# Kernel optimization log

Measured on AMD Instinct MI355X. Metric: run time of the kernel, lower is better.

Reference implementation:

```python
import jax, jax.numpy as jnp
import numpy as np

D = 64       # CNF state dimension
H = 512      # MLP hidden width
B = 8192     # batch


def setup_inputs() -> dict:
    key = jax.random.key(0)
    ks = jax.random.split(key, 8)
    s1 = 1.0 / np.sqrt(D + 1)
    s2 = 1.0 / np.sqrt(H)
    return {
        "t": jax.random.uniform(ks[0], (1,), dtype=jnp.float32),
        "x": jax.random.normal(ks[1], (B, D + 1), dtype=jnp.float32),
        "W1": jax.random.normal(ks[2], (D + 1, H), dtype=jnp.float32) * s1,
        "b1": jnp.zeros((H,), dtype=jnp.float32),
        "W2": jax.random.normal(ks[3], (H, H), dtype=jnp.float32) * s2,
        "b2": jnp.zeros((H,), dtype=jnp.float32),
        "W3": jax.random.normal(ks[4], (H, D), dtype=jnp.float32) * s2,
        "b3": jnp.zeros((D,), dtype=jnp.float32),
    }


def reference(t, x, W1, b1, W2, b2, W3, b3):
    # CNF.forward: strip log-density channel, evaluate vf and its exact divergence.
    xs = x[..., :-1]                      # [B, D]
    tt = t[0]

    def vf_single(xi):                    # xi: [D] -> [D]
        inp = jnp.concatenate([tt[None], xi])          # vf(t*ones, x) with t prepended
        h = jnp.tanh(inp @ W1 + b1)
        h = jnp.tanh(h @ W2 + b2)
        return h @ W3 + b3

    dx = jax.vmap(vf_single)(xs)                        # [B, D]
    # exact divergence: trace of per-sample Jacobian via reverse-mode (matches torch jacrev)
    J = jax.vmap(jax.jacrev(vf_single))(xs)             # [B, D, D]
    div = jnp.trace(J, axis1=-2, axis2=-1)              # [B]
    return jnp.concatenate([dx, div[:, None]], axis=-1) # [B, D+1]
```

## Files before the change

kernel.cpp:

```cpp
#include <hip/hip_runtime.h>

#define HH 512
#define DD 64
#define MROWS 32
#define TPB 512
#define LP 520

typedef unsigned short u16;
typedef short s16x8 __attribute__((ext_vector_type(8)));
typedef float f32x4 __attribute__((ext_vector_type(4)));

#define MFMA16(A,B,C) __builtin_amdgcn_mfma_f32_16x16x32_bf16((A),(B),(C),0,0,0)

#define OFF_EF   0
#define OFF_W2F  (HH*HH)
#define OFF_W1F  (2*HH*HH)
#define OFF_W3F  (2*HH*HH + HH*DD)
#define OFF_Z0B  ((2*HH*HH + 2*HH*DD)*2)

__device__ __forceinline__ u16 f2bf(float f) {
    unsigned u = __builtin_bit_cast(unsigned, f);
    u += 0x7fffu + ((u >> 16) & 1u);
    return (u16)(u >> 16);
}
__device__ __forceinline__ float bf2f(u16 h) {
    return __builtin_bit_cast(float, (unsigned)h << 16);
}
__device__ __forceinline__ float fast_tanh(float x) {
    float e = __expf(2.0f * x);
    return 1.0f - 2.0f * __builtin_amdgcn_rcpf(e + 1.0f);
}

__global__ __launch_bounds__(256) void precompute(
    const float* __restrict__ t,  const float* __restrict__ W1,
    const float* __restrict__ b1, const float* __restrict__ W2,
    const float* __restrict__ W3, u16* __restrict__ ws16, float* __restrict__ z0)
{
    __shared__ float T[16 * 264 > 256 * 20 ? 16 * 264 : 256 * 20];
    u16* Ef  = ws16 + OFF_EF;
    u16* W2f = ws16 + OFF_W2F;
    u16* W1f = ws16 + OFF_W1F;
    u16* W3f = ws16 + OFF_W3F;

    const int bid = blockIdx.x, tid = threadIdx.x;
    const int lane = tid & 63, wv = tid >> 6;
    const int m16 = lane & 15, q = lane >> 4;

    if (bid < 64) {
        const int nt = bid >> 1, bh = bid & 1;
        const int a0 = nt * 16, b0 = bh * 256;
        s16x8 afh[2], afl[2];
#pragma unroll
        for (int h = 0; h < 2; ++h)
#pragma unroll
            for (int j = 0; j < 8; ++j) {
                int i = h * 32 + q * 8 + j;
                float v = W1[(1 + i) * HH + a0 + m16];
                u16 hi = f2bf(v);
                afh[h][j] = (short)hi;
                afl[h][j] = (short)f2bf(v - bf2f(hi));
            }
#pragma unroll
        for (int bt = 0; bt < 4; ++bt) {
            int bl = wv * 64 + bt * 16;
            s16x8 bfh[2], bfl[2];
#pragma unroll
            for (int h = 0; h < 2; ++h) {
                const float* src = W3 + (b0 + bl + m16) * DD + h * 32 + q * 8;
                float4 p0 = *(const float4*)(src);
                float4 p1 = *(const float4*)(src + 4);
                float vv[8] = {p0.x,p0.y,p0.z,p0.w,p1.x,p1.y,p1.z,p1.w};
#pragma unroll
                for (int j = 0; j < 8; ++j) {
                    u16 hi = f2bf(vv[j]);
                    bfh[h][j] = (short)hi;
                    bfl[h][j] = (short)f2bf(vv[j] - bf2f(hi));
                }
            }
            f32x4 c = {0.f, 0.f, 0.f, 0.f};
#pragma unroll
            for (int h = 0; h < 2; ++h) {
                c = MFMA16(afh[h], bfh[h], c);
                c = MFMA16(afh[h], bfl[h], c);
                c = MFMA16(afl[h], bfh[h], c);
            }
#pragma unroll
            for (int r = 0; r < 4; ++r)
                T[(4 * q + r) * 264 + bl + m16] = c[r];
        }
        __syncthreads();
#pragma unroll
        for (int p = 0; p < 2; ++p) {
            int ksl = p * 4 + wv;
            int al  = m16;
            int blc = ksl * 32 + q * 8;
            const float* w2p = W2 + (a0 + al) * HH + b0 + blc;
            float4 wa = *(const float4*)(w2p), wb = *(const float4*)(w2p + 4);
            const float* glp = T + al * 264 + blc;
            s16x8 o;
            o[0]=(short)f2bf(wa.x*glp[0]); o[1]=(short)f2bf(wa.y*glp[1]);
            o[2]=(short)f2bf(wa.z*glp[2]); o[3]=(short)f2bf(wa.w*glp[3]);
            o[4]=(short)f2bf(wb.x*glp[4]); o[5]=(short)f2bf(wb.y*glp[5]);
            o[6]=(short)f2bf(wb.z*glp[6]); o[7]=(short)f2bf(wb.w*glp[7]);
            *(s16x8*)(Ef + nt * 8192 + (b0 / 32 + ksl) * 512 + lane * 8) = o;
        }
        if (bh == 0 && tid < 128) {
            int ks = tid >> 6, ln = tid & 63;
            int n  = nt * 16 + (ln & 15);
            int k0 = ks * 32 + (ln >> 4) * 8;
            s16x8 o;
#pragma unroll
            for (int j = 0; j < 8; ++j) o[j] = (short)f2bf(W1[(1 + k0 + j) * HH + n]);
            *(s16x8*)(W1f + nt * 1024 + ks * 512 + ln * 8) = o;
        }
    } else if (bid < 128) {
        const int nt = (bid - 64) >> 1, kh = (bid - 64) & 1;
        const int n0 = nt * 16, k0 = kh * 256;
#pragma unroll
        for (int it = 0; it < 4; ++it) {
            int r = (tid >> 2) + it * 64;
            int c = (tid & 3) * 4;
            float4 v = *(const float4*)(W2 + (k0 + r) * HH + n0 + c);
            *(float4*)(T + r * 20 + c) = v;
        }
        __syncthreads();
#pragma unroll
        for (int p = 0; p < 2; ++p) {
            int ksl = p * 4 + wv;
            int kq  = ksl * 32 + q * 8;
            s16x8 o;
#pragma unroll
            for (int j = 0; j < 8; ++j) o[j] = (short)f2bf(T[(kq + j) * 20 + m16]);
            *(s16x8*)(W2f + nt * 8192 + (k0 / 32 + ksl) * 512 + lane * 8) = o;
        }
    } else if (bid < 136) {
        const int ot = (bid - 128) >> 1, kh = (bid - 128) & 1;
        const int o0 = ot * 16, k0 = kh * 256;
#pragma unroll
        for (int it = 0; it < 4; ++it) {
            int r = (tid >> 2) + it * 64;
            int c = (tid & 3) * 4;
            float4 v = *(const float4*)(W3 + (k0 + r) * DD + o0 + c);
            *(float4*)(T + r * 20 + c) = v;
        }
        __syncthreads();
#pragma unroll
        for (int p = 0; p < 2; ++p) {
            int ksl = p * 4 + wv;
            int kq  = ksl * 32 + q * 8;
            s16x8 o;
#pragma unroll
            for (int j = 0; j < 8; ++j) o[j] = (short)f2bf(T[(kq + j) * 20 + m16]);
            *(s16x8*)(W3f + ot * 8192 + (k0 / 32 + ksl) * 512 + lane * 8) = o;
        }
    } else {
        for (int n = tid; n < HH; n += 256)
            z0[n] = b1[n] + t[0] * W1[n];
    }
}

__global__ __launch_bounds__(TPB, 2) void cnf_main(
    const float* __restrict__ x,  const u16* __restrict__ ws16,
    const float* __restrict__ z0, const float* __restrict__ b2,
    const float* __restrict__ b3, float* __restrict__ out)
{
    __shared__ u16 h1s[MROWS * LP];
    __shared__ u16 h2s[MROWS * LP];
    __shared__ u16 d2s[MROWS * LP];
    __shared__ float z0s[HH];
    __shared__ float b2s[HH];
    __shared__ float b3s[DD];
    __shared__ float divacc[8][MROWS];

    const u16* Ef  = ws16 + OFF_EF;
    const u16* W2f = ws16 + OFF_W2F;
    const u16* W1f = ws16 + OFF_W1F;
    const u16* W3f = ws16 + OFF_W3F;

    const int tid  = threadIdx.x;
    const int lane = tid & 63;
    const int w    = tid >> 6;
    const int m16  = lane & 15;
    const int q    = lane >> 4;
    const int kq   = q * 8;
    const int r0   = blockIdx.x * MROWS;

    const int noff = (blockIdx.x >> 3) & 31;
    const int koff = (blockIdx.x >> 3) & 15;

    int tile[4];
#pragma unroll
    for (int ct = 0; ct < 4; ++ct) tile[ct] = (4 * w + ct + noff) & 31;

    u16* xs = d2s;

    s16x8 p1b[4][2];
#pragma unroll
    for (int ct = 0; ct < 4; ++ct) {
        const u16* bb = W1f + tile[ct] * 1024 + lane * 8;
        p1b[ct][0] = *(const s16x8*)(bb);
        p1b[ct][1] = *(const s16x8*)(bb + 512);
    }
    const u16* w2bp[4];
#pragma unroll
    for (int ct = 0; ct < 4; ++ct) w2bp[ct] = W2f + tile[ct] * 8192 + lane * 8;
    s16x8 Bv[4][4];
#pragma unroll
    for (int k = 0; k < 4; ++k) {
        const int kk = (koff + k) & 15;
#pragma unroll
        for (int ct = 0; ct < 4; ++ct)
            Bv[k][ct] = *(const s16x8*)(w2bp[ct] + kk * 512);
    }

    for (int idx = tid; idx < MROWS * DD; idx += TPB) {
        int r = idx >> 6, c = idx & 63;
        xs[r * 72 + c] = f2bf(x[(r0 + r) * (DD + 1) + c]);
    }
    if (tid < HH) { z0s[tid] = z0[tid]; b2s[tid] = b2[tid]; }
    if (tid < DD) b3s[tid] = b3[tid];
    __syncthreads();

    float d1reg[2][4][4];

    {
        s16x8 xa[2][2];
#pragma unroll
        for (int rt = 0; rt < 2; ++rt)
#pragma unroll
            for (int h = 0; h < 2; ++h)
                xa[rt][h] = *(const s16x8*)(xs + (rt * 16 + m16) * 72 + h * 32 + kq);
#pragma unroll
        for (int ct = 0; ct < 4; ++ct) {
            const int col = tile[ct] * 16 + m16;
            const float zc = z0s[col];
#pragma unroll
            for (int rt = 0; rt < 2; ++rt) {
                f32x4 c = {0.f, 0.f, 0.f, 0.f};
                c = MFMA16(xa[rt][0], p1b[ct][0], c);
                c = MFMA16(xa[rt][1], p1b[ct][1], c);
#pragma unroll
                for (int i = 0; i < 4; ++i) {
                    float hv = fast_tanh(c[i] + zc);
                    h1s[(rt * 16 + 4 * q + i) * LP + col] = f2bf(hv);
                    d1reg[rt][ct][i] = 1.0f - hv * hv;
                }
            }
        }
    }
    __syncthreads();

    f32x4 acc[2][4];
#pragma unroll
    for (int rt = 0; rt < 2; ++rt)
#pragma unroll
        for (int ct = 0; ct < 4; ++ct) acc[rt][ct] = (f32x4){0.f,0.f,0.f,0.f};
    {
        const u16* ap0 = h1s + m16 * LP + kq;
        const u16* ap1 = h1s + (16 + m16) * LP + kq;
        s16x8 Aq[2][2];
        {
            const int kk0 = koff & 15;
            Aq[0][0] = *(const s16x8*)(ap0 + kk0 * 32);
            Aq[0][1] = *(const s16x8*)(ap1 + kk0 * 32);
        }
#pragma unroll
        for (int ks = 0; ks < 16; ++ks) {
            const int sl = ks & 3, cur = ks & 1;
            if (ks < 15) {
                const int kn = (koff + ks + 1) & 15;
                Aq[cur ^ 1][0] = *(const s16x8*)(ap0 + kn * 32);
                Aq[cur ^ 1][1] = *(const s16x8*)(ap1 + kn * 32);
            }
#pragma unroll
            for (int ct = 0; ct < 4; ++ct) {
                acc[0][ct] = MFMA16(Aq[cur][0], Bv[sl][ct], acc[0][ct]);
                acc[1][ct] = MFMA16(Aq[cur][1], Bv[sl][ct], acc[1][ct]);
            }
            if (ks < 12) {
                const int kn = (koff + ks + 4) & 15;
#pragma unroll
                for (int ct = 0; ct < 4; ++ct)
                    Bv[sl][ct] = *(const s16x8*)(w2bp[ct] + kn * 512);
            }
        }
    }

    const u16* efp[4];
#pragma unroll
    for (int ct = 0; ct < 4; ++ct) efp[ct] = Ef + tile[ct] * 8192 + lane * 8;
    s16x8 Ev[4][4];
#pragma unroll
    for (int k = 0; k < 2; ++k) {
        const int kk = (koff + k) & 15;
#pragma unroll
        for (int ct = 0; ct < 4; ++ct)
            Ev[k][ct] = *(const s16x8*)(efp[ct] + kk * 512);
    }

#pragma unroll
    for (int rt = 0; rt < 2; ++rt)
#pragma unroll
        for (int ct = 0; ct < 4; ++ct) {
            const int col = tile[ct] * 16 + m16;
            const float bc = b2s[col];
#pragma unroll
            for (int i = 0; i < 4; ++i) {
                int row = rt * 16 + 4 * q + i;
                float hv = fast_tanh(acc[rt][ct][i] + bc);
                h2s[row * LP + col] = f2bf(hv);
                d2s[row * LP + col] = f2bf(1.0f - hv * hv);
            }
        }
    __syncthreads();

    {
        const int rowt = w >> 2;
        const int ot   = (w + noff) & 3;
        const u16* ap = h2s + (rowt * 16 + m16) * LP + kq;
        const u16* bp = W3f + ot * 8192 + lane * 8;
        s16x8 W3r[4];
#pragma unroll
        for (int k = 0; k < 4; ++k)
            W3r[k] = *(const s16x8*)(bp + ((koff + k) & 15) * 512);
        f32x4 cA = {0.f,0.f,0.f,0.f}, cB = {0.f,0.f,0.f,0.f};
#pragma unroll
        for (int ks = 0; ks < 16; ++ks) {
            const int kk = (koff + ks) & 15;
            s16x8 f = *(const s16x8*)(ap + kk * 32);
            const int sl = ks & 3;
            if (ks & 1) cB = MFMA16(f, W3r[sl], cB);
            else        cA = MFMA16(f, W3r[sl], cA);
            if (ks < 12) W3r[sl] = *(const s16x8*)(bp + ((koff + ks + 4) & 15) * 512);
        }
        f32x4 c3 = cA + cB;
        const int o = ot * 16 + m16;
#pragma unroll
        for (int i = 0; i < 4; ++i)
            out[(r0 + rowt * 16 + 4 * q + i) * (DD + 1) + o] = c3[i] + b3s[o];
    }

    {
        f32x4 g[2][4];
#pragma unroll
        for (int rt = 0; rt < 2; ++rt)
#pragma unroll
            for (int ct = 0; ct < 4; ++ct) g[rt][ct] = (f32x4){0.f,0.f,0.f,0.f};

#pragma unroll
        for (int k = 2; k < 4; ++k) {
            const int kk = (koff + k) & 15;
#pragma unroll
            for (int ct = 0; ct < 4; ++ct)
                Ev[k][ct] = *(const s16x8*)(efp[ct] + kk * 512);
        }
        const u16* dp0 = d2s + m16 * LP + kq;
        const u16* dp1 = d2s + (16 + m16) * LP + kq;
        s16x8 Aq[2][2];
        {
            const int kk0 = koff & 15;
            Aq[0][0] = *(const s16x8*)(dp0 + kk0 * 32);
            Aq[0][1] = *(const s16x8*)(dp1 + kk0 * 32);
        }
#pragma unroll
        for (int ks = 0; ks < 16; ++ks) {
            const int sl = ks & 3, cur = ks & 1;
            if (ks < 15) {
                const int kn = (koff + ks + 1) & 15;
                Aq[cur ^ 1][0] = *(const s16x8*)(dp0 + kn * 32);
                Aq[cur ^ 1][1] = *(const s16x8*)(dp1 + kn * 32);
            }
#pragma unroll
            for (int ct = 0; ct < 4; ++ct) {
                g[0][ct] = MFMA16(Aq[cur][0], Ev[sl][ct], g[0][ct]);
                g[1][ct] = MFMA16(Aq[cur][1], Ev[sl][ct], g[1][ct]);
            }
            if (ks < 12) {
                const int kn = (koff + ks + 4) & 15;
#pragma unroll
                for (int ct = 0; ct < 4; ++ct)
                    Ev[sl][ct] = *(const s16x8*)(efp[ct] + kn * 512);
            }
        }
#pragma unroll
        for (int rt = 0; rt < 2; ++rt)
#pragma unroll
            for (int i = 0; i < 4; ++i) {
                float v = d1reg[rt][0][i] * g[rt][0][i]
                        + d1reg[rt][1][i] * g[rt][1][i]
                        + d1reg[rt][2][i] * g[rt][2][i]
                        + d1reg[rt][3][i] * g[rt][3][i];
                v += __shfl_xor(v, 1, 64);
                v += __shfl_xor(v, 2, 64);
                v += __shfl_xor(v, 4, 64);
                v += __shfl_xor(v, 8, 64);
                if (m16 == 0) divacc[w][rt * 16 + 4 * q + i] = v;
            }
    }
    __syncthreads();

    if (tid < MROWS) {
        float s = 0.0f;
#pragma unroll
        for (int ww = 0; ww < 8; ++ww) s += divacc[ww][tid];
        out[(r0 + tid) * (DD + 1) + DD] = s;
    }
}

extern "C" void kernel_launch(void* const* d_in, const int* in_sizes, int n_in,
                              void* d_out, int out_size, void* d_ws, size_t ws_size,
                              hipStream_t stream) {
    const float* t  = (const float*)d_in[0];
    const float* x  = (const float*)d_in[1];
    const float* W1 = (const float*)d_in[2];
    const float* b1 = (const float*)d_in[3];
    const float* W2 = (const float*)d_in[4];
    const float* b2 = (const float*)d_in[5];
    const float* W3 = (const float*)d_in[6];
    const float* b3 = (const float*)d_in[7];
    float* out = (float*)d_out;

    u16*   ws16 = (u16*)d_ws;
    float* z0   = (float*)((char*)d_ws + OFF_Z0B);

    precompute<<<137, 256, 0, stream>>>(t, W1, b1, W2, W3, ws16, z0);
    cnf_main<<<8192 / MROWS, TPB, 0, stream>>>(x, ws16, z0, b2, b3, out);
}
```

Before: 92.20 us.

## Double rows per block to reuse W2/E fragments and alias h1/h2 LDS buffers

Each block now handles 64 rows instead of 32, so every W2 and E fragment loaded from global memory feeds four row tiles of MFMAs instead of two. To fit LDS, the h1 and h2 buffers are merged into one, with an extra barrier before h2 overwrites h1. The weight prefetch depth drops from 4 to 3 stages to save registers. The layer-3 GEMM is reassigned so each wave computes two output tiles. The grid halves to 128 blocks, below the GPU's CU count, and register pressure rises with the larger accumulator and d1 arrays. Both risk lower occupancy and load imbalance.

```diff
diff --git a/kernel.cpp b/kernel.cpp
--- a/kernel.cpp
+++ b/kernel.cpp
@@ -2,11 +2,13 @@
 
 #define HH 512
 #define DD 64
-#define MROWS 32
+#define MROWS 64
 #define TPB 512
+#define NBLK (8192 / MROWS)
 #define LP 520
 
 typedef unsigned short u16;
+typedef unsigned int u32;
 typedef short s16x8 __attribute__((ext_vector_type(8)));
 typedef float f32x4 __attribute__((ext_vector_type(4)));
 
@@ -164,8 +166,7 @@
     const float* __restrict__ z0, const float* __restrict__ b2,
     const float* __restrict__ b3, float* __restrict__ out)
 {
-    __shared__ u16 h1s[MROWS * LP];
-    __shared__ u16 h2s[MROWS * LP];
+    __shared__ u16 h12s[MROWS * LP];
     __shared__ u16 d2s[MROWS * LP];
     __shared__ float z0s[HH];
     __shared__ float b2s[HH];
@@ -204,9 +205,9 @@
     const u16* w2bp[4];
 #pragma unroll
     for (int ct = 0; ct < 4; ++ct) w2bp[ct] = W2f + tile[ct] * 8192 + lane * 8;
-    s16x8 Bv[4][4];
-#pragma unroll
-    for (int k = 0; k < 4; ++k) {
+    s16x8 Bv[3][4];
+#pragma unroll
+    for (int k = 0; k < 3; ++k) {
         const int kk = (koff + k) & 15;
 #pragma unroll
         for (int ct = 0; ct < 4; ++ct)
@@ -217,16 +218,17 @@
         int r = idx >> 6, c = idx & 63;
         xs[r * 72 + c] = f2bf(x[(r0 + r) * (DD + 1) + c]);
     }
-    if (tid < HH) { z0s[tid] = z0[tid]; b2s[tid] = b2[tid]; }
+    z0s[tid] = z0[tid];
+    b2s[tid] = b2[tid];
     if (tid < DD) b3s[tid] = b3[tid];
     __syncthreads();
 
-    float d1reg[2][4][4];
+    float d1reg[4][4][4];
 
     {
-        s16x8 xa[2][2];
-#pragma unroll
-        for (int rt = 0; rt < 2; ++rt)
+        s16x8 xa[4][2];
+#pragma unroll
+        for (int rt = 0; rt < 4; ++rt)
 #pragma unroll
             for (int h = 0; h < 2; ++h)
                 xa[rt][h] = *(const s16x8*)(xs + (rt * 16 + m16) * 72 + h * 32 + kq);
@@ -235,14 +237,14 @@
             const int col = tile[ct] * 16 + m16;
             const float zc = z0s[col];
 #pragma unroll
-            for (int rt = 0; rt < 2; ++rt) {
+            for (int rt = 0; rt < 4; ++rt) {
                 f32x4 c = {0.f, 0.f, 0.f, 0.f};
                 c = MFMA16(xa[rt][0], p1b[ct][0], c);
                 c = MFMA16(xa[rt][1], p1b[ct][1], c);
 #pragma unroll
                 for (int i = 0; i < 4; ++i) {
                     float hv = fast_tanh(c[i] + zc);
-                    h1s[(rt * 16 + 4 * q + i) * LP + col] = f2bf(hv);
+                    h12s[(rt * 16 + 4 * q + i) * LP + col] = f2bf(hv);
                     d1reg[rt][ct][i] = 1.0f - hv * hv;
                 }
             }
@@ -250,35 +252,38 @@
     }
     __syncthreads();
 
-    f32x4 acc[2][4];
-#pragma unroll
-    for (int rt = 0; rt < 2; ++rt)
+    f32x4 acc[4][4];
+#pragma unroll
+    for (int rt = 0; rt < 4; ++rt)
 #pragma unroll
         for (int ct = 0; ct < 4; ++ct) acc[rt][ct] = (f32x4){0.f,0.f,0.f,0.f};
     {
-        const u16* ap0 = h1s + m16 * LP + kq;
-        const u16* ap1 = h1s + (16 + m16) * LP + kq;
-        s16x8 Aq[2][2];
+        const u16* ap[4];
+#pragma unroll
+        for (int rt = 0; rt < 4; ++rt) ap[rt] = h12s + (rt * 16 + m16) * LP + kq;
+        s16x8 Aq[2][4];
         {
             const int kk0 = koff & 15;
-            Aq[0][0] = *(const s16x8*)(ap0 + kk0 * 32);
-            Aq[0][1] = *(const s16x8*)(ap1 + kk0 * 32);
+#pragma unroll
+            for (int rt = 0; rt < 4; ++rt)
+                Aq[0][rt] = *(const s16x8*)(ap[rt] + kk0 * 32);
         }
 #pragma unroll
         for (int ks = 0; ks < 16; ++ks) {
-            const int sl = ks & 3, cur = ks & 1;
+            const int sl = ks % 3, cur = ks & 1;
             if (ks < 15) {
                 const int kn = (koff + ks + 1) & 15;
-                Aq[cur ^ 1][0] = *(const s16x8*)(ap0 + kn * 32);
-                Aq[cur ^ 1][1] = *(const s16x8*)(ap1 + kn * 32);
-            }
-#pragma unroll
-            for (int ct = 0; ct < 4; ++ct) {
-                acc[0][ct] = MFMA16(Aq[cur][0], Bv[sl][ct], acc[0][ct]);
-                acc[1][ct] = MFMA16(Aq[cur][1], Bv[sl][ct], acc[1][ct]);
-            }
-            if (ks < 12) {
-                const int kn = (koff + ks + 4) & 15;
+#pragma unroll
+                for (int rt = 0; rt < 4; ++rt)
+                    Aq[cur ^ 1][rt] = *(const s16x8*)(ap[rt] + kn * 32);
+            }
+#pragma unroll
+            for (int ct = 0; ct < 4; ++ct)
+#pragma unroll
+                for (int rt = 0; rt < 4; ++rt)
+                    acc[rt][ct] = MFMA16(Aq[cur][rt], Bv[sl][ct], acc[rt][ct]);
+            if (ks < 13) {
+                const int kn = (koff + ks + 3) & 15;
 #pragma unroll
                 for (int ct = 0; ct < 4; ++ct)
                     Bv[sl][ct] = *(const s16x8*)(w2bp[ct] + kn * 512);
@@ -289,7 +294,7 @@
     const u16* efp[4];
 #pragma unroll
     for (int ct = 0; ct < 4; ++ct) efp[ct] = Ef + tile[ct] * 8192 + lane * 8;
-    s16x8 Ev[4][4];
+    s16x8 Ev[3][4];
 #pragma unroll
     for (int k = 0; k < 2; ++k) {
         const int kk = (koff + k) & 15;
@@ -298,8 +303,10 @@
             Ev[k][ct] = *(const s16x8*)(efp[ct] + kk * 512);
     }
 
-#pragma unroll
-    for (int rt = 0; rt < 2; ++rt)
+    __syncthreads();
+
+#pragma unroll
+    for (int rt = 0; rt < 4; ++rt)
 #pragma unroll
         for (int ct = 0; ct < 4; ++ct) {
             const int col = tile[ct] * 16 + m16;
@@ -308,82 +315,96 @@
             for (int i = 0; i < 4; ++i) {
                 int row = rt * 16 + 4 * q + i;
                 float hv = fast_tanh(acc[rt][ct][i] + bc);
-                h2s[row * LP + col] = f2bf(hv);
+                h12s[row * LP + col] = f2bf(hv);
                 d2s[row * LP + col] = f2bf(1.0f - hv * hv);
             }
         }
     __syncthreads();
 
     {
-        const int rowt = w >> 2;
-        const int ot   = (w + noff) & 3;
-        const u16* ap = h2s + (rowt * 16 + m16) * LP + kq;
-        const u16* bp = W3f + ot * 8192 + lane * 8;
-        s16x8 W3r[4];
-#pragma unroll
-        for (int k = 0; k < 4; ++k)
-            W3r[k] = *(const s16x8*)(bp + ((koff + k) & 15) * 512);
-        f32x4 cA = {0.f,0.f,0.f,0.f}, cB = {0.f,0.f,0.f,0.f};
+        const int rowt = w >> 1;
+        const int ot0  = (((2 * w    ) & 3) + noff) & 3;
+        const int ot1  = (((2 * w + 1) & 3) + noff) & 3;
+        const u16* ap3 = h12s + (rowt * 16 + m16) * LP + kq;
+        const u16* bp0 = W3f + ot0 * 8192 + lane * 8;
+        const u16* bp1 = W3f + ot1 * 8192 + lane * 8;
+        s16x8 R0[4], R1[4];
+#pragma unroll
+        for (int k = 0; k < 4; ++k) {
+            const int kk = (koff + k) & 15;
+            R0[k] = *(const s16x8*)(bp0 + kk * 512);
+            R1[k] = *(const s16x8*)(bp1 + kk * 512);
+        }
+        f32x4 c0 = {0.f,0.f,0.f,0.f}, c1 = {0.f,0.f,0.f,0.f};
 #pragma unroll
         for (int ks = 0; ks < 16; ++ks) {
             const int kk = (koff + ks) & 15;
-            s16x8 f = *(const s16x8*)(ap + kk * 32);
+            s16x8 f = *(const s16x8*)(ap3 + kk * 32);
             const int sl = ks & 3;
-            if (ks & 1) cB = MFMA16(f, W3r[sl], cB);
-            else        cA = MFMA16(f, W3r[sl], cA);
-            if (ks < 12) W3r[sl] = *(const s16x8*)(bp + ((koff + ks + 4) & 15) * 512);
-        }
-        f32x4 c3 = cA + cB;
-        const int o = ot * 16 + m16;
-#pragma unroll
-        for (int i = 0; i < 4; ++i)
-            out[(r0 + rowt * 16 + 4 * q + i) * (DD + 1) + o] = c3[i] + b3s[o];
+            c0 = MFMA16(f, R0[sl], c0);
+            c1 = MFMA16(f, R1[sl], c1);
+            if (ks < 12) {
+                const int kn = (koff + ks + 4) & 15;
+                R0[sl] = *(const s16x8*)(bp0 + kn * 512);
+                R1[sl] = *(const s16x8*)(bp1 + kn * 512);
+            }
+        }
+        const int o0c = ot0 * 16 + m16;
+        const int o1c = ot1 * 16 + m16;
+#pragma unroll
+        for (int i = 0; i < 4; ++i) {
+            const int row = r0 + rowt * 16 + 4 * q + i;
+            out[row * (DD + 1) + o0c] = c0[i] + b3s[o0c];
+            out[row * (DD + 1) + o1c] = c1[i] + b3s[o1c];
+        }
     }
 
     {
-        f32x4 g[2][4];
-#pragma unroll
-        for (int rt = 0; rt < 2; ++rt)
+        f32x4 g[4][4];
+#pragma unroll
+        for (int rt = 0; rt < 4; ++rt)
 #pragma unroll
             for (int ct = 0; ct < 4; ++ct) g[rt][ct] = (f32x4){0.f,0.f,0.f,0.f};
 
-#pragma unroll
-        for (int k = 2; k < 4; ++k) {
-            const int kk = (koff + k) & 15;
+        {
+            const int kk = (koff + 2) & 15;
 #pragma unroll
             for (int ct = 0; ct < 4; ++ct)
-                Ev[k][ct] = *(const s16x8*)(efp[ct] + kk * 512);
-        }
-        const u16* dp0 = d2s + m16 * LP + kq;
-        const u16* dp1 = d2s + (16 + m16) * LP + kq;
-        s16x8 Aq[2][2];
+                Ev[2][ct] = *(const s16x8*)(efp[ct] + kk * 512);
+        }
+        const u16* dp[4];
+#pragma unroll
+        for (int rt = 0; rt < 4; ++rt) dp[rt] = d2s + (rt * 16 + m16) * LP + kq;
+        s16x8 Aq[2][4];
         {
             const int kk0 = koff & 15;
-            Aq[0][0] = *(const s16x8*)(dp0 + kk0 * 32);
-            Aq[0][1] = *(const s16x8*)(dp1 + kk0 * 32);
+#pragma unroll
+            for (int rt = 0; rt < 4; ++rt)
+                Aq[0][rt] = *(const s16x8*)(dp[rt] + kk0 * 32);
         }
 #pragma unroll
         for (int ks = 0; ks < 16; ++ks) {
-            const int sl = ks & 3, cur = ks & 1;
+            const int sl = ks % 3, cur = ks & 1;
             if (ks < 15) {
                 const int kn = (koff + ks + 1) & 15;
-                Aq[cur ^ 1][0] = *(const s16x8*)(dp0 + kn * 32);
-                Aq[cur ^ 1][1] = *(const s16x8*)(dp1 + kn * 32);
-            }
-#pragma unroll
-            for (int ct = 0; ct < 4; ++ct) {
-                g[0][ct] = MFMA16(Aq[cur][0], Ev[sl][ct], g[0][ct]);
-                g[1][ct] = MFMA16(Aq[cur][1], Ev[sl][ct], g[1][ct]);
-            }
-            if (ks < 12) {
-                const int kn = (koff + ks + 4) & 15;
+#pragma unroll
+                for (int rt = 0; rt < 4; ++rt)
+                    Aq[cur ^ 1][rt] = *(const s16x8*)(dp[rt] + kn * 32);
+            }
+#pragma unroll
+            for (int ct = 0; ct < 4; ++ct)
+#pragma unroll
+                for (int rt = 0; rt < 4; ++rt)
+                    g[rt][ct] = MFMA16(Aq[cur][rt], Ev[sl][ct], g[rt][ct]);
+            if (ks < 13) {
+                const int kn = (koff + ks + 3) & 15;
 #pragma unroll
                 for (int ct = 0; ct < 4; ++ct)
                     Ev[sl][ct] = *(const s16x8*)(efp[ct] + kn * 512);
             }
         }
 #pragma unroll
-        for (int rt = 0; rt < 2; ++rt)
+        for (int rt = 0; rt < 4; ++rt)
 #pragma unroll
             for (int i = 0; i < 4; ++i) {
                 float v = d1reg[rt][0][i] * g[rt][0][i]
@@ -424,5 +445,5 @@
     float* z0   = (float*)((char*)d_ws + OFF_Z0B);
 
     precompute<<<137, 256, 0, stream>>>(t, W1, b1, W2, W3, ws16, z0);
-    cnf_main<<<8192 / MROWS, TPB, 0, stream>>>(x, ws16, z0, b2, b3, out);
-}
+    cnf_main<<<NBLK, TPB, 0, stream>>>(x, ws16, z0, b2, b3, out);
+}
```

Result: slower. 99.84 us (+8.3%).

## Stream W2 and E tiles via global_load_lds double-buffered staging

Applied to the files above, without the earlier changes.

Replaces register-prefetched W2 and E B-operand loads with per-wave asynchronous global-to-LDS DMA into a two-slot staging buffer, synchronised with explicit vmcnt and lgkmcnt waits. It also merges the h1 and h2 LDS buffers, preloads all of W3 into registers before the layer-2 epilogue, and moves the output GEMM after the divergence GEMM. It drops the per-block column-tile rotation. The aim is to cut register pressure and hide global load latency behind the MFMA work. In exchange it adds about 64KB of LDS staging, which may limit occupancy to one block per CU, and relies on hand-placed wait counts being correct.

```diff
diff --git a/kernel.cpp b/kernel.cpp
--- a/kernel.cpp
+++ b/kernel.cpp
@@ -29,6 +29,23 @@
 __device__ __forceinline__ float fast_tanh(float x) {
     float e = __expf(2.0f * x);
     return 1.0f - 2.0f * __builtin_amdgcn_rcpf(e + 1.0f);
+}
+
+template<int N> __device__ __forceinline__ void wait_vmcnt() {
+    asm volatile("s_waitcnt vmcnt(%0)" :: "n"(N) : "memory");
+}
+__device__ __forceinline__ void wait_lgkm0() {
+    asm volatile("s_waitcnt lgkmcnt(0)" ::: "memory");
+}
+__device__ __forceinline__ void dma16(const u16* g, u16* l) {
+    __builtin_amdgcn_global_load_lds(
+        (const __attribute__((address_space(1))) void*)g,
+        (__attribute__((address_space(3))) void*)l, 16, 0, 0);
+}
+__device__ __forceinline__ void issue4(const u16* base, int kk, u16* dst) {
+#pragma unroll
+    for (int ct = 0; ct < 4; ++ct)
+        dma16(base + ct * 8192 + kk * 512, dst + ct * 512);
 }
 
 __global__ __launch_bounds__(256) void precompute(
@@ -164,9 +181,9 @@
     const float* __restrict__ z0, const float* __restrict__ b2,
     const float* __restrict__ b3, float* __restrict__ out)
 {
-    __shared__ u16 h1s[MROWS * LP];
-    __shared__ u16 h2s[MROWS * LP];
+    __shared__ u16 h12s[MROWS * LP];
     __shared__ u16 d2s[MROWS * LP];
+    __shared__ u16 Bst[8][2][2048];
     __shared__ float z0s[HH];
     __shared__ float b2s[HH];
     __shared__ float b3s[DD];
@@ -185,39 +202,29 @@
     const int kq   = q * 8;
     const int r0   = blockIdx.x * MROWS;
 
-    const int noff = (blockIdx.x >> 3) & 31;
     const int koff = (blockIdx.x >> 3) & 15;
 
-    int tile[4];
-#pragma unroll
-    for (int ct = 0; ct < 4; ++ct) tile[ct] = (4 * w + ct + noff) & 31;
-
     u16* xs = d2s;
 
+    const u16* w2b = W2f + (4 * w) * 8192 + lane * 8;
+    const u16* efb = Ef  + (4 * w) * 8192 + lane * 8;
+    u16* st0 = &Bst[w][0][0];
+    u16* st1 = &Bst[w][1][0];
+
     s16x8 p1b[4][2];
 #pragma unroll
     for (int ct = 0; ct < 4; ++ct) {
-        const u16* bb = W1f + tile[ct] * 1024 + lane * 8;
+        const u16* bb = W1f + (4 * w + ct) * 1024 + lane * 8;
         p1b[ct][0] = *(const s16x8*)(bb);
         p1b[ct][1] = *(const s16x8*)(bb + 512);
-    }
-    const u16* w2bp[4];
-#pragma unroll
-    for (int ct = 0; ct < 4; ++ct) w2bp[ct] = W2f + tile[ct] * 8192 + lane * 8;
-    s16x8 Bv[4][4];
-#pragma unroll
-    for (int k = 0; k < 4; ++k) {
-        const int kk = (koff + k) & 15;
-#pragma unroll
-        for (int ct = 0; ct < 4; ++ct)
-            Bv[k][ct] = *(const s16x8*)(w2bp[ct] + kk * 512);
     }
 
     for (int idx = tid; idx < MROWS * DD; idx += TPB) {
         int r = idx >> 6, c = idx & 63;
         xs[r * 72 + c] = f2bf(x[(r0 + r) * (DD + 1) + c]);
     }
-    if (tid < HH) { z0s[tid] = z0[tid]; b2s[tid] = b2[tid]; }
+    z0s[tid] = z0[tid];
+    b2s[tid] = b2[tid];
     if (tid < DD) b3s[tid] = b3[tid];
     __syncthreads();
 
@@ -232,7 +239,7 @@
                 xa[rt][h] = *(const s16x8*)(xs + (rt * 16 + m16) * 72 + h * 32 + kq);
 #pragma unroll
         for (int ct = 0; ct < 4; ++ct) {
-            const int col = tile[ct] * 16 + m16;
+            const int col = (4 * w + ct) * 16 + m16;
             const float zc = z0s[col];
 #pragma unroll
             for (int rt = 0; rt < 2; ++rt) {
@@ -242,12 +249,15 @@
 #pragma unroll
                 for (int i = 0; i < 4; ++i) {
                     float hv = fast_tanh(c[i] + zc);
-                    h1s[(rt * 16 + 4 * q + i) * LP + col] = f2bf(hv);
+                    h12s[(rt * 16 + 4 * q + i) * LP + col] = f2bf(hv);
                     d1reg[rt][ct][i] = 1.0f - hv * hv;
                 }
             }
         }
     }
+
+    issue4(w2b, (koff + 0) & 15, st0);
+    issue4(w2b, (koff + 1) & 15, st1);
     __syncthreads();
 
     f32x4 acc[2][4];
@@ -256,89 +266,61 @@
 #pragma unroll
         for (int ct = 0; ct < 4; ++ct) acc[rt][ct] = (f32x4){0.f,0.f,0.f,0.f};
     {
-        const u16* ap0 = h1s + m16 * LP + kq;
-        const u16* ap1 = h1s + (16 + m16) * LP + kq;
-        s16x8 Aq[2][2];
-        {
-            const int kk0 = koff & 15;
-            Aq[0][0] = *(const s16x8*)(ap0 + kk0 * 32);
-            Aq[0][1] = *(const s16x8*)(ap1 + kk0 * 32);
-        }
+        const u16* ap0 = h12s + m16 * LP + kq;
+        const u16* ap1 = h12s + (16 + m16) * LP + kq;
 #pragma unroll
         for (int ks = 0; ks < 16; ++ks) {
-            const int sl = ks & 3, cur = ks & 1;
-            if (ks < 15) {
-                const int kn = (koff + ks + 1) & 15;
-                Aq[cur ^ 1][0] = *(const s16x8*)(ap0 + kn * 32);
-                Aq[cur ^ 1][1] = *(const s16x8*)(ap1 + kn * 32);
-            }
-#pragma unroll
-            for (int ct = 0; ct < 4; ++ct) {
-                acc[0][ct] = MFMA16(Aq[cur][0], Bv[sl][ct], acc[0][ct]);
-                acc[1][ct] = MFMA16(Aq[cur][1], Bv[sl][ct], acc[1][ct]);
-            }
-            if (ks < 12) {
-                const int kn = (koff + ks + 4) & 15;
-#pragma unroll
-                for (int ct = 0; ct < 4; ++ct)
-                    Bv[sl][ct] = *(const s16x8*)(w2bp[ct] + kn * 512);
-            }
-        }
-    }
-
-    const u16* efp[4];
-#pragma unroll
-    for (int ct = 0; ct < 4; ++ct) efp[ct] = Ef + tile[ct] * 8192 + lane * 8;
-    s16x8 Ev[4][4];
-#pragma unroll
-    for (int k = 0; k < 2; ++k) {
-        const int kk = (koff + k) & 15;
-#pragma unroll
-        for (int ct = 0; ct < 4; ++ct)
-            Ev[k][ct] = *(const s16x8*)(efp[ct] + kk * 512);
-    }
+            if (ks < 15) wait_vmcnt<4>(); else wait_vmcnt<0>();
+            u16* sb = (ks & 1) ? st1 : st0;
+            const u16* bb = sb + lane * 8;
+            s16x8 b0v = *(const s16x8*)(bb);
+            s16x8 b1v = *(const s16x8*)(bb + 512);
+            s16x8 b2v = *(const s16x8*)(bb + 1024);
+            s16x8 b3v = *(const s16x8*)(bb + 1536);
+            const int kk = (koff + ks) & 15;
+            s16x8 a0 = *(const s16x8*)(ap0 + kk * 32);
+            s16x8 a1 = *(const s16x8*)(ap1 + kk * 32);
+            wait_lgkm0();
+            if (ks < 14) issue4(w2b, (koff + ks + 2) & 15, sb);
+            acc[0][0] = MFMA16(a0, b0v, acc[0][0]);
+            acc[1][0] = MFMA16(a1, b0v, acc[1][0]);
+            acc[0][1] = MFMA16(a0, b1v, acc[0][1]);
+            acc[1][1] = MFMA16(a1, b1v, acc[1][1]);
+            acc[0][2] = MFMA16(a0, b2v, acc[0][2]);
+            acc[1][2] = MFMA16(a1, b2v, acc[1][2]);
+            acc[0][3] = MFMA16(a0, b3v, acc[0][3]);
+            acc[1][3] = MFMA16(a1, b3v, acc[1][3]);
+        }
+    }
+
+    const int rowt = w >> 2;
+    const int ot   = w & 3;
+    const u16* bp3 = W3f + ot * 8192 + lane * 8;
+    s16x8 W3pre[16];
+#pragma unroll
+    for (int k = 0; k < 16; ++k)
+        W3pre[k] = *(const s16x8*)(bp3 + ((koff + k) & 15) * 512);
+
+    issue4(efb, (koff + 0) & 15, st0);
+    issue4(efb, (koff + 1) & 15, st1);
+
+    __syncthreads();
 
 #pragma unroll
     for (int rt = 0; rt < 2; ++rt)
 #pragma unroll
         for (int ct = 0; ct < 4; ++ct) {
-            const int col = tile[ct] * 16 + m16;
+            const int col = (4 * w + ct) * 16 + m16;
             const float bc = b2s[col];
 #pragma unroll
             for (int i = 0; i < 4; ++i) {
                 int row = rt * 16 + 4 * q + i;
                 float hv = fast_tanh(acc[rt][ct][i] + bc);
-                h2s[row * LP + col] = f2bf(hv);
+                h12s[row * LP + col] = f2bf(hv);
                 d2s[row * LP + col] = f2bf(1.0f - hv * hv);
             }
         }
     __syncthreads();
-
-    {
-        const int rowt = w >> 2;
-        const int ot   = (w + noff) & 3;
-        const u16* ap = h2s + (rowt * 16 + m16) * LP + kq;
-        const u16* bp = W3f + ot * 8192 + lane * 8;
-        s16x8 W3r[4];
-#pragma unroll
-        for (int k = 0; k < 4; ++k)
-            W3r[k] = *(const s16x8*)(bp + ((koff + k) & 15) * 512);
-        f32x4 cA = {0.f,0.f,0.f,0.f}, cB = {0.f,0.f,0.f,0.f};
-#pragma unroll
-        for (int ks = 0; ks < 16; ++ks) {
-            const int kk = (koff + ks) & 15;
-            s16x8 f = *(const s16x8*)(ap + kk * 32);
-            const int sl = ks & 3;
-            if (ks & 1) cB = MFMA16(f, W3r[sl], cB);
-            else        cA = MFMA16(f, W3r[sl], cA);
-            if (ks < 12) W3r[sl] = *(const s16x8*)(bp + ((koff + ks + 4) & 15) * 512);
-        }
-        f32x4 c3 = cA + cB;
-        const int o = ot * 16 + m16;
-#pragma unroll
-        for (int i = 0; i < 4; ++i)
-            out[(r0 + rowt * 16 + 4 * q + i) * (DD + 1) + o] = c3[i] + b3s[o];
-    }
 
     {
         f32x4 g[2][4];
@@ -346,41 +328,30 @@
         for (int rt = 0; rt < 2; ++rt)
 #pragma unroll
             for (int ct = 0; ct < 4; ++ct) g[rt][ct] = (f32x4){0.f,0.f,0.f,0.f};
-
-#pragma unroll
-        for (int k = 2; k < 4; ++k) {
-            const int kk = (koff + k) & 15;
-#pragma unroll
-            for (int ct = 0; ct < 4; ++ct)
-                Ev[k][ct] = *(const s16x8*)(efp[ct] + kk * 512);
-        }
         const u16* dp0 = d2s + m16 * LP + kq;
         const u16* dp1 = d2s + (16 + m16) * LP + kq;
-        s16x8 Aq[2][2];
-        {
-            const int kk0 = koff & 15;
-            Aq[0][0] = *(const s16x8*)(dp0 + kk0 * 32);
-            Aq[0][1] = *(const s16x8*)(dp1 + kk0 * 32);
-        }
 #pragma unroll
         for (int ks = 0; ks < 16; ++ks) {
-            const int sl = ks & 3, cur = ks & 1;
-            if (ks < 15) {
-                const int kn = (koff + ks + 1) & 15;
-                Aq[cur ^ 1][0] = *(const s16x8*)(dp0 + kn * 32);
-                Aq[cur ^ 1][1] = *(const s16x8*)(dp1 + kn * 32);
-            }
-#pragma unroll
-            for (int ct = 0; ct < 4; ++ct) {
-                g[0][ct] = MFMA16(Aq[cur][0], Ev[sl][ct], g[0][ct]);
-                g[1][ct] = MFMA16(Aq[cur][1], Ev[sl][ct], g[1][ct]);
-            }
-            if (ks < 12) {
-                const int kn = (koff + ks + 4) & 15;
-#pragma unroll
-                for (int ct = 0; ct < 4; ++ct)
-                    Ev[sl][ct] = *(const s16x8*)(efp[ct] + kn * 512);
-            }
+            if (ks < 15) wait_vmcnt<4>(); else wait_vmcnt<0>();
+            u16* sb = (ks & 1) ? st1 : st0;
+            const u16* bb = sb + lane * 8;
+            s16x8 e0 = *(const s16x8*)(bb);
+            s16x8 e1 = *(const s16x8*)(bb + 512);
+            s16x8 e2 = *(const s16x8*)(bb + 1024);
+            s16x8 e3 = *(const s16x8*)(bb + 1536);
+            const int kk = (koff + ks) & 15;
+            s16x8 a0 = *(const s16x8*)(dp0 + kk * 32);
+            s16x8 a1 = *(const s16x8*)(dp1 + kk * 32);
+            wait_lgkm0();
+            if (ks < 14) issue4(efb, (koff + ks + 2) & 15, sb);
+            g[0][0] = MFMA16(a0, e0, g[0][0]);
+            g[1][0] = MFMA16(a1, e0, g[1][0]);
+            g[0][1] = MFMA16(a0, e1, g[0][1]);
+            g[1][1] = MFMA16(a1, e1, g[1][1]);
+            g[0][2] = MFMA16(a0, e2, g[0][2]);
+            g[1][2] = MFMA16(a1, e2, g[1][2]);
+            g[0][3] = MFMA16(a0, e3, g[0][3]);
+            g[1][3] = MFMA16(a1, e3, g[1][3]);
         }
 #pragma unroll
         for (int rt = 0; rt < 2; ++rt)
@@ -396,6 +367,22 @@
                 v += __shfl_xor(v, 8, 64);
                 if (m16 == 0) divacc[w][rt * 16 + 4 * q + i] = v;
             }
+    }
+
+    {
+        const u16* ap3 = h12s + (rowt * 16 + m16) * LP + kq;
+        f32x4 cA = {0.f,0.f,0.f,0.f}, cB = {0.f,0.f,0.f,0.f};
+#pragma unroll
+        for (int ks = 0; ks < 16; ++ks) {
+            s16x8 f = *(const s16x8*)(ap3 + ((koff + ks) & 15) * 32);
+            if (ks & 1) cB = MFMA16(f, W3pre[ks], cB);
+            else        cA = MFMA16(f, W3pre[ks], cA);
+        }
+        f32x4 c3 = cA + cB;
+        const int o = ot * 16 + m16;
+#pragma unroll
+        for (int i = 0; i < 4; ++i)
+            out[(r0 + rowt * 16 + 4 * q + i) * (DD + 1) + o] = c3[i] + b3s[o];
     }
     __syncthreads();
 
```

New measurement: 93.42 us. About the same (+1.3%).
